# Optimization experiments

Hardware: AMD Instinct MI355X
Metric: run time of the kernel (lower is better)

Reference implementation:

```python
import jax, jax.numpy as jnp
import numpy as np

D_MODEL = 1024
NUM_HEADS = 16
D_INTERNAL = D_MODEL // NUM_HEADS
ROPE_BASE = 10000.0


def justnorm(x):
    return x / jnp.linalg.norm(x, axis=-1, keepdims=True)


def rotate_half(x):
    h = x.shape[-1] // 2
    return jnp.concatenate([-x[..., h:], x[..., :h]], axis=-1)


def setup_inputs() -> dict:
    key = jax.random.key(0)
    ks = jax.random.split(key, 8)
    B, T, dm, H, di = 4, 2048, D_MODEL, NUM_HEADS, D_INTERNAL
    x = jax.random.normal(ks[0], (B, T, dm), dtype=jnp.float32)
    stdev_h = 1.0 / (dm + di) ** 0.5
    qkv = jax.random.uniform(ks[1], (H, 3 * di, dm), minval=-stdev_h, maxval=stdev_h, dtype=jnp.float32)
    qkv = justnorm(qkv)  # per-row L2 normalization as in torch init
    sqk = (dm ** -0.5) * jnp.ones((H, di), dtype=jnp.float32)
    stdev = 1.0 / (4 * dm + dm) ** 0.5
    W_O = justnorm(jax.random.uniform(ks[2], (dm, dm), minval=-stdev, maxval=stdev, dtype=jnp.float32))
    Wu = justnorm(jax.random.uniform(ks[3], (8 * dm, dm), minval=-stdev, maxval=stdev, dtype=jnp.float32))
    Wv = justnorm(jax.random.uniform(ks[4], (dm, 4 * dm), minval=-stdev, maxval=stdev, dtype=jnp.float32))
    attn_alpha = (dm ** -0.5) * jnp.ones((dm,), dtype=jnp.float32)
    mlp_alpha = jnp.ones((dm,), dtype=jnp.float32)
    suv = jnp.ones((8 * dm,), dtype=jnp.float32)
    return {"x": x, "qkv": qkv, "sqk": sqk, "W_O": W_O, "Wu": Wu, "Wv": Wv,
            "attn_alpha": attn_alpha, "mlp_alpha": mlp_alpha, "suv": suv}


def _forward(x, qkv, sqk, W_O, Wu, Wv, attn_alpha, mlp_alpha, suv):
    B, T, dm = x.shape
    H = qkv.shape[0]
    di = qkv.shape[1] // 3
    sqrt_dm = jnp.sqrt(jnp.asarray(dm, x.dtype))
    # Per-head QKV projection, batched over heads: [B,H,T,3*di]
    qkv_out = jnp.einsum('btd,hed->bhte', x, qkv)
    Q, K, V = jnp.split(qkv_out, 3, axis=-1)
    # RoPE over full d_internal
    inv_freq = 1.0 / (ROPE_BASE ** (jnp.arange(0, di, 2, dtype=jnp.float32) / di))
    freqs = jnp.arange(T, dtype=jnp.float32)[:, None] * inv_freq[None, :]
    emb = jnp.concatenate([freqs, freqs], axis=-1)  # [T, di]
    cos, sin = jnp.cos(emb), jnp.sin(emb)
    Q = Q * cos + rotate_half(Q) * sin
    K = K * cos + rotate_half(K) * sin
    # sqk effective scale: sqk * (1.0 / d_model**-0.5)
    sqk_eff = sqk * sqrt_dm  # [H, di]
    Q = justnorm(Q) * sqk_eff[None, :, None, :]
    K = justnorm(K) * sqk_eff[None, :, None, :]
    # SDPA with non-standard scale = d_model**0.5, causal (eval mode)
    scores = jnp.einsum('bhqd,bhkd->bhqk', Q, K) * sqrt_dm
    causal = jnp.tril(jnp.ones((T, T), dtype=bool))
    scores = jnp.where(causal[None, None], scores, jnp.finfo(x.dtype).min)
    attn = jax.nn.softmax(scores, axis=-1)
    out = jnp.einsum('bhqk,bhkd->bhqd', attn, V)
    t = out.transpose(0, 2, 1, 3).reshape(B, T, dm)
    t = t @ W_O.T
    # nGPT-style attention lerp residual: attn_alpha * (0.05 / d_model**-0.5)
    lr = jnp.abs(attn_alpha * (0.05 * sqrt_dm))
    A = justnorm(x)
    Bn = justnorm(t)
    x1 = justnorm(A + lr * (Bn - A))
    # SwiGLU MLP
    uv = x1 @ Wu.T
    uv = (suv * sqrt_dm) * uv
    tn = justnorm(uv)
    u, v = jnp.split(tn, 2, axis=-1)
    res = u * jax.nn.silu(v)
    t = res @ Wv.T
    lr2 = jnp.abs(mlp_alpha * 0.05)
    A = justnorm(x1)
    Bn = justnorm(t)
    return justnorm(A + lr2 * (Bn - A))


def reference(x, qkv, sqk, W_O, Wu, Wv, attn_alpha, mlp_alpha, suv):
    return _forward(x, qkv, sqk, W_O, Wu, Wv, attn_alpha, mlp_alpha, suv)
```

## Files before the change

### kernel.cpp

```cpp
#include <hip/hip_runtime.h>
#include <hip/hip_bf16.h>


#define B_   4
#define T_   2048
#define DM   1024
#define H_   16
#define DI   64
#define NROW (B_ * T_)

using bf16 = __hip_bfloat16;
typedef __attribute__((ext_vector_type(8))) short bfrag;
typedef __attribute__((ext_vector_type(4))) float f4;

#define EXPB 46.166241f

__device__ __forceinline__ float ldf(const float* p) { return *p; }
__device__ __forceinline__ float ldf(const bf16* p)  { return __bfloat162float(*p); }
__device__ __forceinline__ void  stf(float* p, float v) { *p = v; }
__device__ __forceinline__ void  stf(bf16* p, float v)  { *p = __float2bfloat16(v); }

__device__ __forceinline__ unsigned short bfbits(float a) {
    bf16 h = __float2bfloat16(a);
    return __builtin_bit_cast(unsigned short, h);
}
__device__ __forceinline__ unsigned pk2(float a, float b) {
    return (unsigned)bfbits(a) | ((unsigned)bfbits(b) << 16);
}

__device__ __forceinline__ float fexp2(float x) {
    return __builtin_amdgcn_exp2f(x);
}

__device__ __forceinline__ float wave_sum(float v) {
#pragma unroll
    for (int off = 32; off; off >>= 1) v += __shfl_xor(v, off, 64);
    return v;
}

__device__ __forceinline__ float block_sum(float v) {
    __shared__ float sm[4];
    int lane = threadIdx.x & 63, w = threadIdx.x >> 6;
    v = wave_sum(v);
    __syncthreads();
    if (lane == 0) sm[w] = v;
    __syncthreads();
    return sm[0] + sm[1] + sm[2] + sm[3];
}

typedef __attribute__((address_space(1))) const void g_void;
typedef __attribute__((address_space(3))) void l_void;
__device__ __forceinline__ void gl_lds(const void* g, void* l) {
    __builtin_amdgcn_global_load_lds((g_void*)g, (l_void*)l, 16, 0, 0);
}

__global__ __launch_bounds__(256)
void f32_to_bf16_k(const float* __restrict__ in, bf16* __restrict__ out, long n)
{
    long i = ((long)blockIdx.x * 256 + threadIdx.x) * 8;
    if (i >= n) return;
    float4 a = *(const float4*)(in + i);
    float4 b = *(const float4*)(in + i + 4);
    union { bfrag f; unsigned u[4]; } o;
    o.u[0] = pk2(a.x, a.y); o.u[1] = pk2(a.z, a.w);
    o.u[2] = pk2(b.x, b.y); o.u[3] = pk2(b.z, b.w);
    *(bfrag*)(out + i) = o.f;
}

template <typename TC>
__global__ __launch_bounds__(256)
void gemm_bf16(const bf16* __restrict__ A, const bf16* __restrict__ Bm,
               TC* __restrict__ C, int M, int N, int K)
{
    __shared__ bf16 lds[2][2][128 * 32];
    const int tid  = threadIdx.x;
    const int w    = tid >> 6, lane = tid & 63;
    const int g    = lane >> 4, c = lane & 15;
    const int m0   = blockIdx.y * 128, n0 = blockIdx.x * 128;
    const int wm   = w >> 1, wn = w & 1;

    const int srow = (lane >> 2);
    const int skc  = 8 * (lane & 3);

    f4 acc[4][4] = {{{0,0,0,0}}};

    const int NT = K >> 5;

#pragma unroll
    for (int q = 0; q < 2; q++) {
        int cidx = w * 2 + q;
        int row  = 16 * cidx + srow;
        gl_lds(A + (long)(m0 + row) * K + skc, &lds[0][0][cidx * 512]);
        gl_lds(Bm + (long)(n0 + row) * K + skc, &lds[0][1][cidx * 512]);
    }
    __syncthreads();

    for (int t = 0; t < NT; t++) {
        int cur = t & 1;
        if (t + 1 < NT) {
            int k0 = (t + 1) << 5;
#pragma unroll
            for (int q = 0; q < 2; q++) {
                int cidx = w * 2 + q;
                int row  = 16 * cidx + srow;
                gl_lds(A + (long)(m0 + row) * K + k0 + skc, &lds[cur ^ 1][0][cidx * 512]);
                gl_lds(Bm + (long)(n0 + row) * K + k0 + skc, &lds[cur ^ 1][1][cidx * 512]);
            }
        }
        const bf16* bufA = &lds[cur][0][0];
        const bf16* bufB = &lds[cur][1][0];
        bfrag af[4], bb[4];
#pragma unroll
        for (int mi = 0; mi < 4; mi++)
            af[mi] = *(const bfrag*)(bufA + (64 * wm + 16 * mi + c) * 32 + 8 * g);
#pragma unroll
        for (int ni = 0; ni < 4; ni++)
            bb[ni] = *(const bfrag*)(bufB + (64 * wn + 16 * ni + c) * 32 + 8 * g);
#pragma unroll
        for (int mi = 0; mi < 4; mi++)
#pragma unroll
            for (int ni = 0; ni < 4; ni++)
                acc[mi][ni] = __builtin_amdgcn_mfma_f32_16x16x32_bf16(
                    af[mi], bb[ni], acc[mi][ni], 0, 0, 0);
        __syncthreads();
    }

#pragma unroll
    for (int mi = 0; mi < 4; mi++)
#pragma unroll
        for (int ni = 0; ni < 4; ni++) {
            long row = m0 + 64 * wm + 16 * mi + 4 * g;
            long col = n0 + 64 * wn + 16 * ni + c;
#pragma unroll
            for (int r = 0; r < 4; r++)
                stf(&C[(row + r) * N + col], acc[mi][ni][r]);
        }
}

template <typename TC>
__global__ __launch_bounds__(512, 2)
void gemm_bf16_256(const bf16* __restrict__ A, const bf16* __restrict__ Bm,
                   TC* __restrict__ C, int M, int N, int K)
{
    __shared__ bf16 lds[2][2][256 * 64];
    const int tid  = threadIdx.x;
    const int w    = tid >> 6, lane = tid & 63;
    const int g    = lane >> 4, c = lane & 15;
    const int m0   = blockIdx.y * 256, n0 = blockIdx.x * 256;
    const int wm   = w & 1, wn = w >> 1;
    const int srow8 = lane >> 3;
    const int swz   = 8 * ((lane & 7) ^ srow8);
    const int cx    = c & 7;

    f4 acc[8][4] = {{{0,0,0,0}}};

    const int NT = K >> 6;

    auto STAGE = [&](int buf, int t) {
        int k0 = t << 6;
#pragma unroll
        for (int i = 0; i < 4; i++) {
            int rb = w * 32 + i * 8;
            gl_lds(A  + (long)(m0 + rb + srow8) * K + k0 + swz, &lds[buf][0][rb * 64]);
            gl_lds(Bm + (long)(n0 + rb + srow8) * K + k0 + swz, &lds[buf][1][rb * 64]);
        }
    };

    STAGE(0, 0);
    STAGE(1, 1);
    asm volatile("s_waitcnt vmcnt(8)" ::: "memory");
    __builtin_amdgcn_s_barrier();

    for (int t = 0; t < NT; t++) {
        const bf16* bufA = &lds[t & 1][0][0];
        const bf16* bufB = &lds[t & 1][1][0];

        bfrag a0[4][2], b0[4][2];
#pragma unroll
        for (int mi = 0; mi < 4; mi++)
#pragma unroll
            for (int kk = 0; kk < 2; kk++)
                a0[mi][kk] = *(const bfrag*)(bufA + (wm * 128 + mi * 16 + c) * 64
                                                  + 8 * ((4 * kk + g) ^ cx));
#pragma unroll
        for (int ni = 0; ni < 4; ni++)
#pragma unroll
            for (int kk = 0; kk < 2; kk++)
                b0[ni][kk] = *(const bfrag*)(bufB + (wn * 64 + ni * 16 + c) * 64
                                                  + 8 * ((4 * kk + g) ^ cx));
        asm volatile("s_waitcnt lgkmcnt(0)" ::: "memory");
        __builtin_amdgcn_sched_barrier(0);
        __builtin_amdgcn_s_setprio(1);
#pragma unroll
        for (int mi = 0; mi < 4; mi++)
#pragma unroll
            for (int ni = 0; ni < 4; ni++) {
                acc[mi][ni] = __builtin_amdgcn_mfma_f32_16x16x32_bf16(
                    a0[mi][0], b0[ni][0], acc[mi][ni], 0, 0, 0);
                acc[mi][ni] = __builtin_amdgcn_mfma_f32_16x16x32_bf16(
                    a0[mi][1], b0[ni][1], acc[mi][ni], 0, 0, 0);
            }
        __builtin_amdgcn_s_setprio(0);

        bfrag a1[4][2];
#pragma unroll
        for (int mi = 0; mi < 4; mi++)
#pragma unroll
            for (int kk = 0; kk < 2; kk++)
                a1[mi][kk] = *(const bfrag*)(bufA + (wm * 128 + (mi + 4) * 16 + c) * 64
                                                  + 8 * ((4 * kk + g) ^ cx));
        asm volatile("s_waitcnt lgkmcnt(0)" ::: "memory");
        __builtin_amdgcn_sched_barrier(0);
        __builtin_amdgcn_s_setprio(1);
#pragma unroll
        for (int mi = 0; mi < 4; mi++)
#pragma unroll
            for (int ni = 0; ni < 4; ni++) {
                acc[mi + 4][ni] = __builtin_amdgcn_mfma_f32_16x16x32_bf16(
                    a1[mi][0], b0[ni][0], acc[mi + 4][ni], 0, 0, 0);
                acc[mi + 4][ni] = __builtin_amdgcn_mfma_f32_16x16x32_bf16(
                    a1[mi][1], b0[ni][1], acc[mi + 4][ni], 0, 0, 0);
            }
        __builtin_amdgcn_s_setprio(0);

        __builtin_amdgcn_s_barrier();
        if (t + 2 < NT) {
            STAGE(t & 1, t + 2);
            asm volatile("s_waitcnt vmcnt(8)" ::: "memory");
        } else if (t + 1 < NT) {
            asm volatile("s_waitcnt vmcnt(0)" ::: "memory");
        }
        __builtin_amdgcn_s_barrier();
    }

#pragma unroll
    for (int mi = 0; mi < 8; mi++)
#pragma unroll
        for (int ni = 0; ni < 4; ni++) {
            long row = m0 + wm * 128 + mi * 16 + 4 * g;
            long col = n0 + wn * 64 + ni * 16 + c;
#pragma unroll
            for (int r = 0; r < 4; r++)
                stf(&C[(row + r) * N + col], acc[mi][ni][r]);
        }
}

__global__ __launch_bounds__(256)
void rope_norm_qk(const bf16* __restrict__ QKVb, const float* __restrict__ sqk,
                  bf16* __restrict__ Qb, bf16* __restrict__ Kb, bf16* __restrict__ Vt)
{
    int gw   = (blockIdx.x * 256 + threadIdx.x) >> 6;
    int lane = threadIdx.x & 63;
    int h = gw / NROW, row = gw % NROW, t = row % T_, b = row / T_;

    const bf16* base = QKVb + (long)row * 3072 + h * 192;
    float q = __bfloat162float(base[lane]);
    float k = __bfloat162float(base[64 + lane]);
    bf16  v = base[128 + lane];

    int   j   = lane & 31;
    float inv = expf(-(float)j * (9.210340371976184f / 32.f));
    float ang = (float)t * inv;
    float s = sinf(ang), cc = cosf(ang);

    float qp = __shfl_xor(q, 32, 64);
    float kp = __shfl_xor(k, 32, 64);
    float sgn = (lane < 32) ? -1.f : 1.f;
    float qr = q * cc + sgn * qp * s;
    float kr = k * cc + sgn * kp * s;

    float qs = wave_sum(qr * qr);
    float ks = wave_sum(kr * kr);
    float se = sqk[h * 64 + lane] * 32.f;

    long idx = ((long)h * NROW + row) * 64 + lane;
    Qb[idx] = __float2bfloat16(qr * rsqrtf(qs) * se * EXPB);
    Kb[idx] = __float2bfloat16(kr * rsqrtf(ks) * se);
    Vt[((long)(h * B_ + b) * 64 + lane) * T_ + t] = v;
}

__global__ __launch_bounds__(256)
void attn_mfma(const bf16* __restrict__ Qb, const bf16* __restrict__ Kb,
               const bf16* __restrict__ Vt, bf16* __restrict__ O)
{
    __shared__ bf16 kv[2][2][64 * 64];

    int orig   = blockIdx.x;
    int xcd    = orig & 7;
    int rest   = orig >> 3;
    int bh     = xcd * 8 + (rest & 7);
    int blkraw = rest >> 3;
    int blk    = (blkraw & 1) ? (15 - (blkraw >> 1)) : (blkraw >> 1);
    int w      = threadIdx.x >> 6;
    int pr     = blk * 4 + w;
    int h = bh >> 2, b = bh & 3;

    int lane = threadIdx.x & 63;
    int g = lane >> 4, c = lane & 15;

    const bf16* kbase = Kb + ((long)h * NROW + (long)b * T_) * 64;
    const bf16* vbase = Vt + (long)(h * B_ + b) * 64 * (long)T_;

    int q0A = pr * 16, q0B = (127 - pr) * 16;
    const bf16* qbA = Qb + ((long)h * NROW + (long)b * T_ + q0A) * 64;
    const bf16* qbB = Qb + ((long)h * NROW + (long)b * T_ + q0B) * 64;
    bfrag qfA0 = *(const bfrag*)(qbA + (long)c * 64 + 8 * g);
    bfrag qfA1 = *(const bfrag*)(qbA + (long)c * 64 + 32 + 8 * g);
    bfrag qfB0 = *(const bfrag*)(qbB + (long)c * 64 + 8 * g);
    bfrag qfB1 = *(const bfrag*)(qbB + (long)c * 64 + 32 + 8 * g);

    const f4 CINIT = {-EXPB, -EXPB, -EXPB, -EXPB};

    f4 otA[4] = {{0,0,0,0},{0,0,0,0},{0,0,0,0},{0,0,0,0}};
    f4 otB[4] = {{0,0,0,0},{0,0,0,0},{0,0,0,0},{0,0,0,0}};
    float lA = 0.f, lB = 0.f;

    const int nA = blk, nB = 31 - blk, KT = nB;
    int qgA = q0A + c, qgB = q0B + c;

    const int srow8  = lane >> 3;
    const int swz    = 8 * ((lane & 7) ^ srow8);

    auto STAGE = [&](int buf, int kt) {
        int k0 = kt * 64;
#pragma unroll
        for (int i = 0; i < 2; i++) {
            int rb  = (w * 2 + i) * 8;
            int row = rb + srow8;
            gl_lds(kbase + (long)(k0 + row) * 64 + swz, &kv[buf][0][rb * 64]);
            gl_lds(vbase + (long)row * T_ + k0 + swz,   &kv[buf][1][rb * 64]);
        }
    };

    STAGE(0, 0);
    __syncthreads();

    const int cx = c & 7;

    for (int kt = 0; kt <= KT; kt++) {
        int buf = kt & 1;
        if (kt < KT) STAGE(buf ^ 1, kt + 1);

        const bf16* Kl = &kv[buf][0][0];
        const bf16* Vl = &kv[buf][1][0];
        int k0 = kt * 64;
        bool actA = (kt <= nA);
        unsigned wvA[8], wvB[8];

#pragma unroll
        for (int kb = 0; kb < 4; kb++) {
            const bf16* kr = Kl + (16 * kb + c) * 64;
            bfrag ka = *(const bfrag*)(kr + 8 * (g ^ cx));
            bfrag kc = *(const bfrag*)(kr + 8 * ((g | 4) ^ cx));

            f4 sB = __builtin_amdgcn_mfma_f32_16x16x32_bf16(ka, qfB0, CINIT, 0, 0, 0);
            sB = __builtin_amdgcn_mfma_f32_16x16x32_bf16(kc, qfB1, sB, 0, 0, 0);
            if (kt == nB) {
#pragma unroll
                for (int r = 0; r < 4; r++)
                    if (k0 + 16 * kb + 4 * g + r > qgB) sB[r] = -1e30f;
            }
            float eB0 = fexp2(sB[0]), eB1 = fexp2(sB[1]);
            float eB2 = fexp2(sB[2]), eB3 = fexp2(sB[3]);
            lB += (eB0 + eB1) + (eB2 + eB3);
            wvB[2 * kb]     = pk2(eB0, eB1);
            wvB[2 * kb + 1] = pk2(eB2, eB3);

            if (actA) {
                f4 sA = __builtin_amdgcn_mfma_f32_16x16x32_bf16(ka, qfA0, CINIT, 0, 0, 0);
                sA = __builtin_amdgcn_mfma_f32_16x16x32_bf16(kc, qfA1, sA, 0, 0, 0);
                if (kt == nA) {
#pragma unroll
                    for (int r = 0; r < 4; r++)
                        if (k0 + 16 * kb + 4 * g + r > qgA) sA[r] = -1e30f;
                }
                float eA0 = fexp2(sA[0]), eA1 = fexp2(sA[1]);
                float eA2 = fexp2(sA[2]), eA3 = fexp2(sA[3]);
                lA += (eA0 + eA1) + (eA2 + eA3);
                wvA[2 * kb]     = pk2(eA0, eA1);
                wvA[2 * kb + 1] = pk2(eA2, eA3);
            }
        }

#pragma unroll
        for (int p = 0; p < 2; p++) {
            int s0l = c + 32 * (g & 1), s1l = s0l + 16;
            bool hi = (g >= 2);

            unsigned Bb0 = (unsigned)__shfl((int)wvB[4 * p + 0], s0l, 64);
            unsigned Bb1 = (unsigned)__shfl((int)wvB[4 * p + 1], s0l, 64);
            unsigned Bb2 = (unsigned)__shfl((int)wvB[4 * p + 2], s0l, 64);
            unsigned Bb3 = (unsigned)__shfl((int)wvB[4 * p + 3], s0l, 64);
            unsigned Bb4 = (unsigned)__shfl((int)wvB[4 * p + 0], s1l, 64);
            unsigned Bb5 = (unsigned)__shfl((int)wvB[4 * p + 1], s1l, 64);
            unsigned Bb6 = (unsigned)__shfl((int)wvB[4 * p + 2], s1l, 64);
            unsigned Bb7 = (unsigned)__shfl((int)wvB[4 * p + 3], s1l, 64);
            union { bfrag f; unsigned u[4]; } pfB;
            pfB.u[0] = hi ? Bb2 : Bb0;
            pfB.u[1] = hi ? Bb3 : Bb1;
            pfB.u[2] = hi ? Bb6 : Bb4;
            pfB.u[3] = hi ? Bb7 : Bb5;

            union { bfrag f; unsigned u[4]; } pfA;
            if (actA) {
                unsigned Ab0 = (unsigned)__shfl((int)wvA[4 * p + 0], s0l, 64);
                unsigned Ab1 = (unsigned)__shfl((int)wvA[4 * p + 1], s0l, 64);
                unsigned Ab2 = (unsigned)__shfl((int)wvA[4 * p + 2], s0l, 64);
                unsigned Ab3 = (unsigned)__shfl((int)wvA[4 * p + 3], s0l, 64);
                unsigned Ab4 = (unsigned)__shfl((int)wvA[4 * p + 0], s1l, 64);
                unsigned Ab5 = (unsigned)__shfl((int)wvA[4 * p + 1], s1l, 64);
                unsigned Ab6 = (unsigned)__shfl((int)wvA[4 * p + 2], s1l, 64);
                unsigned Ab7 = (unsigned)__shfl((int)wvA[4 * p + 3], s1l, 64);
                pfA.u[0] = hi ? Ab2 : Ab0;
                pfA.u[1] = hi ? Ab3 : Ab1;
                pfA.u[2] = hi ? Ab6 : Ab4;
                pfA.u[3] = hi ? Ab7 : Ab5;
            }

#pragma unroll
            for (int dblk = 0; dblk < 4; dblk++) {
                bfrag vf = *(const bfrag*)(Vl + (16 * dblk + c) * 64
                                              + 8 * (((p << 2) | g) ^ cx));
                otB[dblk] = __builtin_amdgcn_mfma_f32_16x16x32_bf16(vf, pfB.f, otB[dblk], 0, 0, 0);
                if (actA)
                    otA[dblk] = __builtin_amdgcn_mfma_f32_16x16x32_bf16(vf, pfA.f, otA[dblk], 0, 0, 0);
            }
        }
        __syncthreads();
    }

    lA += __shfl_xor(lA, 16, 64); lA += __shfl_xor(lA, 32, 64);
    lB += __shfl_xor(lB, 16, 64); lB += __shfl_xor(lB, 32, 64);

    float invA = 1.f / lA, invB = 1.f / lB;
    long orowA = (long)(b * T_ + q0A + c) * DM + h * 64;
    long orowB = (long)(b * T_ + q0B + c) * DM + h * 64;
#pragma unroll
    for (int dblk = 0; dblk < 4; dblk++)
#pragma unroll
        for (int r = 0; r < 4; r++) {
            O[orowA + 16 * dblk + 4 * g + r] = __float2bfloat16(otA[dblk][r] * invA);
            O[orowB + 16 * dblk + 4 * g + r] = __float2bfloat16(otB[dblk][r] * invB);
        }
}

template <typename TT>
__global__ __launch_bounds__(256)
void lerp_norm(const float* __restrict__ X, const TT* __restrict__ Tt,
               const float* __restrict__ alpha, float ascale,
               float* __restrict__ Out, bf16* __restrict__ OutB)
{
    long row = blockIdx.x;
    const float* xr = X  + row * DM;
    const TT*    tr = Tt + row * DM;
    int tid = threadIdx.x;

    float xs[4], ts[4], sx = 0.f, st = 0.f;
#pragma unroll
    for (int i = 0; i < 4; i++) {
        int d = tid + 256 * i;
        xs[i] = xr[d]; ts[i] = ldf(&tr[d]);
        sx += xs[i] * xs[i]; st += ts[i] * ts[i];
    }
    sx = block_sum(sx);
    st = block_sum(st);
    float ix = rsqrtf(sx), it = rsqrtf(st);

    float ys[4], sy = 0.f;
#pragma unroll
    for (int i = 0; i < 4; i++) {
        int d = tid + 256 * i;
        float a  = xs[i] * ix;
        float bn = ts[i] * it;
        float lr = fabsf(alpha[d] * ascale);
        ys[i] = a + lr * (bn - a);
        sy += ys[i] * ys[i];
    }
    sy = block_sum(sy);
    float iy = rsqrtf(sy);
#pragma unroll
    for (int i = 0; i < 4; i++) {
        int d = tid + 256 * i;
        float o = ys[i] * iy;
        Out[row * DM + d] = o;
        if (OutB) OutB[row * DM + d] = __float2bfloat16(o);
    }
}

__global__ __launch_bounds__(256)
void mlp_act(const bf16* __restrict__ UV, const float* __restrict__ suv,
             bf16* __restrict__ R)
{
    long row = blockIdx.x;
    const bf16* ur = UV + row * 8192;
    int tid = threadIdx.x;

    float ss = 0.f;
#pragma unroll
    for (int i = 0; i < 32; i++) {
        int j = tid + 256 * i;
        float v = __bfloat162float(ur[j]) * suv[j] * 32.f;
        ss += v * v;
    }
    ss = block_sum(ss);
    float inv = rsqrtf(ss);

#pragma unroll
    for (int i = 0; i < 16; i++) {
        int j = tid + 256 * i;
        float u = __bfloat162float(ur[j])        * suv[j]        * 32.f * inv;
        float v = __bfloat162float(ur[4096 + j]) * suv[4096 + j] * 32.f * inv;
        float sil = v / (1.f + __expf(-v));
        R[row * 4096 + j] = __float2bfloat16(u * sil);
    }
}

extern "C" void kernel_launch(void* const* d_in, const int* in_sizes, int n_in,
                              void* d_out, int out_size, void* d_ws, size_t ws_size,
                              hipStream_t stream)
{
    const float* x          = (const float*)d_in[0];
    const float* qkv_w      = (const float*)d_in[1];
    const float* sqk        = (const float*)d_in[2];
    const float* W_O        = (const float*)d_in[3];
    const float* Wu         = (const float*)d_in[4];
    const float* Wv         = (const float*)d_in[5];
    const float* attn_alpha = (const float*)d_in[6];
    const float* mlp_alpha  = (const float*)d_in[7];
    const float* suv        = (const float*)d_in[8];
    float* out = (float*)d_out;

    const long MiB = 1048576;
    char* ws = (char*)d_ws;
    float* x1    = (float*)(ws + 0 * MiB);
    bf16*  x1b   = (bf16*) (ws + 32 * MiB);
    bf16*  QKVb  = (bf16*) (ws + 48 * MiB);
    bf16*  tbuf  = (bf16*) (ws + 48 * MiB);
    bf16*  uv    = (bf16*) (ws + 48 * MiB);
    bf16*  t2    = (bf16*) (ws + 48 * MiB);
    bf16*  xb    = (bf16*) (ws + 144 * MiB);
    bf16*  Qb    = (bf16*) (ws + 144 * MiB);
    bf16*  Wub   = (bf16*) (ws + 144 * MiB);
    bf16*  Kb    = (bf16*) (ws + 160 * MiB);
    bf16*  Vt    = (bf16*) (ws + 176 * MiB);
    bf16*  Wvb   = (bf16*) (ws + 176 * MiB);
    bf16*  res   = (bf16*) (ws + 112 * MiB);
    bf16*  qkvwb = (bf16*) (ws + 192 * MiB);
    bf16*  attno = (bf16*) (ws + 192 * MiB);
    bf16*  Wob   = (bf16*) (ws + 208 * MiB);

    f32_to_bf16_k<<<4096, 256, 0, stream>>>(x, xb, 8388608L);
    f32_to_bf16_k<<<1536, 256, 0, stream>>>(qkv_w, qkvwb, 3145728L);
    f32_to_bf16_k<<<512,  256, 0, stream>>>(W_O, Wob, 1048576L);

    gemm_bf16_256<bf16><<<dim3(12, 32), 512, 0, stream>>>(xb, qkvwb, QKVb, NROW, 3072, DM);

    rope_norm_qk<<<(H_ * NROW) / 4, 256, 0, stream>>>(QKVb, sqk, Qb, Kb, Vt);

    attn_mfma<<<1024, 256, 0, stream>>>(Qb, Kb, Vt, attno);

    gemm_bf16<bf16><<<dim3(8, 64), 256, 0, stream>>>(attno, Wob, tbuf, NROW, DM, DM);

    lerp_norm<bf16><<<NROW, 256, 0, stream>>>(x, tbuf, attn_alpha, 1.6f, x1, x1b);

    f32_to_bf16_k<<<4096, 256, 0, stream>>>(Wu, Wub, 8388608L);
    f32_to_bf16_k<<<2048, 256, 0, stream>>>(Wv, Wvb, 4194304L);

    for (int half = 0; half < 2; half++) {
        gemm_bf16_256<bf16><<<dim3(32, 16), 512, 0, stream>>>(
            x1b + (long)half * 4096 * DM, Wub, uv, 4096, 8 * DM, DM);
        mlp_act<<<4096, 256, 0, stream>>>(uv, suv, res + (long)half * 4096 * 4096);
    }

    gemm_bf16<bf16><<<dim3(8, 64), 256, 0, stream>>>(res, Wvb, t2, NROW, DM, 4 * DM);

    lerp_norm<bf16><<<NROW, 256, 0, stream>>>(x1, t2, mlp_alpha, 0.05f, out, (bf16*)nullptr);
}
```

Before: 581.9 us.

## Interleave attention query-tile assignment across warps and drop fp32 x1 buffer

Attention blocks now assign each warp a query pair strided by 16 instead of four adjacent pairs. Each warp gets its own A/B causal limits, the block loops to the longest warp's limit, and MFMA work is skipped for warps past their range, aiming to balance work across blocks. Separately, the first lerp_norm no longer writes a fp32 x1 buffer, and the final lerp_norm reads the bf16 x1b copy instead, cutting memory traffic. The cost is some precision loss in the residual path, plus idle warps inside a block when limits differ.

```diff
diff --git a/kernel.cpp b/kernel.cpp
--- a/kernel.cpp
+++ b/kernel.cpp
@@ -289,10 +289,9 @@
     int xcd    = orig & 7;
     int rest   = orig >> 3;
     int bh     = xcd * 8 + (rest & 7);
-    int blkraw = rest >> 3;
-    int blk    = (blkraw & 1) ? (15 - (blkraw >> 1)) : (blkraw >> 1);
+    int j      = rest >> 3;
     int w      = threadIdx.x >> 6;
-    int pr     = blk * 4 + w;
+    int pr     = j + 16 * w;
     int h = bh >> 2, b = bh & 3;
 
     int lane = threadIdx.x & 63;
@@ -315,7 +314,9 @@
     f4 otB[4] = {{0,0,0,0},{0,0,0,0},{0,0,0,0},{0,0,0,0}};
     float lA = 0.f, lB = 0.f;
 
-    const int nA = blk, nB = 31 - blk, KT = nB;
+    const int nA = pr >> 2;
+    const int nB = 31 - nA;
+    const int KTblk = 31 - (j >> 2);
     int qgA = q0A + c, qgB = q0B + c;
 
     const int srow8  = lane >> 3;
@@ -337,93 +338,99 @@
 
     const int cx = c & 7;
 
-    for (int kt = 0; kt <= KT; kt++) {
+    for (int kt = 0; kt <= KTblk; kt++) {
         int buf = kt & 1;
-        if (kt < KT) STAGE(buf ^ 1, kt + 1);
+        if (kt < KTblk) STAGE(buf ^ 1, kt + 1);
 
         const bf16* Kl = &kv[buf][0][0];
         const bf16* Vl = &kv[buf][1][0];
         int k0 = kt * 64;
         bool actA = (kt <= nA);
+        bool actB = (kt <= nB);
         unsigned wvA[8], wvB[8];
 
-#pragma unroll
-        for (int kb = 0; kb < 4; kb++) {
-            const bf16* kr = Kl + (16 * kb + c) * 64;
-            bfrag ka = *(const bfrag*)(kr + 8 * (g ^ cx));
-            bfrag kc = *(const bfrag*)(kr + 8 * ((g | 4) ^ cx));
-
-            f4 sB = __builtin_amdgcn_mfma_f32_16x16x32_bf16(ka, qfB0, CINIT, 0, 0, 0);
-            sB = __builtin_amdgcn_mfma_f32_16x16x32_bf16(kc, qfB1, sB, 0, 0, 0);
-            if (kt == nB) {
-#pragma unroll
-                for (int r = 0; r < 4; r++)
-                    if (k0 + 16 * kb + 4 * g + r > qgB) sB[r] = -1e30f;
+        if (actB || actA) {
+#pragma unroll
+            for (int kb = 0; kb < 4; kb++) {
+                const bf16* kr = Kl + (16 * kb + c) * 64;
+                bfrag ka = *(const bfrag*)(kr + 8 * (g ^ cx));
+                bfrag kc = *(const bfrag*)(kr + 8 * ((g | 4) ^ cx));
+
+                if (actB) {
+                    f4 sB = __builtin_amdgcn_mfma_f32_16x16x32_bf16(ka, qfB0, CINIT, 0, 0, 0);
+                    sB = __builtin_amdgcn_mfma_f32_16x16x32_bf16(kc, qfB1, sB, 0, 0, 0);
+                    if (kt == nB) {
+#pragma unroll
+                        for (int r = 0; r < 4; r++)
+                            if (k0 + 16 * kb + 4 * g + r > qgB) sB[r] = -1e30f;
+                    }
+                    float eB0 = fexp2(sB[0]), eB1 = fexp2(sB[1]);
+                    float eB2 = fexp2(sB[2]), eB3 = fexp2(sB[3]);
+                    lB += (eB0 + eB1) + (eB2 + eB3);
+                    wvB[2 * kb]     = pk2(eB0, eB1);
+                    wvB[2 * kb + 1] = pk2(eB2, eB3);
+                }
+
+                if (actA) {
+                    f4 sA = __builtin_amdgcn_mfma_f32_16x16x32_bf16(ka, qfA0, CINIT, 0, 0, 0);
+                    sA = __builtin_amdgcn_mfma_f32_16x16x32_bf16(kc, qfA1, sA, 0, 0, 0);
+                    if (kt == nA) {
+#pragma unroll
+                        for (int r = 0; r < 4; r++)
+                            if (k0 + 16 * kb + 4 * g + r > qgA) sA[r] = -1e30f;
+                    }
+                    float eA0 = fexp2(sA[0]), eA1 = fexp2(sA[1]);
+                    float eA2 = fexp2(sA[2]), eA3 = fexp2(sA[3]);
+                    lA += (eA0 + eA1) + (eA2 + eA3);
+                    wvA[2 * kb]     = pk2(eA0, eA1);
+                    wvA[2 * kb + 1] = pk2(eA2, eA3);
+                }
             }
-            float eB0 = fexp2(sB[0]), eB1 = fexp2(sB[1]);
-            float eB2 = fexp2(sB[2]), eB3 = fexp2(sB[3]);
-            lB += (eB0 + eB1) + (eB2 + eB3);
-            wvB[2 * kb]     = pk2(eB0, eB1);
-            wvB[2 * kb + 1] = pk2(eB2, eB3);
-
-            if (actA) {
-                f4 sA = __builtin_amdgcn_mfma_f32_16x16x32_bf16(ka, qfA0, CINIT, 0, 0, 0);
-                sA = __builtin_amdgcn_mfma_f32_16x16x32_bf16(kc, qfA1, sA, 0, 0, 0);
-                if (kt == nA) {
-#pragma unroll
-                    for (int r = 0; r < 4; r++)
-                        if (k0 + 16 * kb + 4 * g + r > qgA) sA[r] = -1e30f;
+
+#pragma unroll
+            for (int p = 0; p < 2; p++) {
+                int s0l = c + 32 * (g & 1), s1l = s0l + 16;
+                bool hi = (g >= 2);
+
+                union { bfrag f; unsigned u[4]; } pfB, pfA;
+                if (actB) {
+                    unsigned Bb0 = (unsigned)__shfl((int)wvB[4 * p + 0], s0l, 64);
+                    unsigned Bb1 = (unsigned)__shfl((int)wvB[4 * p + 1], s0l, 64);
+                    unsigned Bb2 = (unsigned)__shfl((int)wvB[4 * p + 2], s0l, 64);
+                    unsigned Bb3 = (unsigned)__shfl((int)wvB[4 * p + 3], s0l, 64);
+                    unsigned Bb4 = (unsigned)__shfl((int)wvB[4 * p + 0], s1l, 64);
+                    unsigned Bb5 = (unsigned)__shfl((int)wvB[4 * p + 1], s1l, 64);
+                    unsigned Bb6 = (unsigned)__shfl((int)wvB[4 * p + 2], s1l, 64);
+                    unsigned Bb7 = (unsigned)__shfl((int)wvB[4 * p + 3], s1l, 64);
+                    pfB.u[0] = hi ? Bb2 : Bb0;
+                    pfB.u[1] = hi ? Bb3 : Bb1;
+                    pfB.u[2] = hi ? Bb6 : Bb4;
+                    pfB.u[3] = hi ? Bb7 : Bb5;
                 }
-                float eA0 = fexp2(sA[0]), eA1 = fexp2(sA[1]);
-                float eA2 = fexp2(sA[2]), eA3 = fexp2(sA[3]);
-                lA += (eA0 + eA1) + (eA2 + eA3);
-                wvA[2 * kb]     = pk2(eA0, eA1);
-                wvA[2 * kb + 1] = pk2(eA2, eA3);
-            }
-        }
-
-#pragma unroll
-        for (int p = 0; p < 2; p++) {
-            int s0l = c + 32 * (g & 1), s1l = s0l + 16;
-            bool hi = (g >= 2);
-
-            unsigned Bb0 = (unsigned)__shfl((int)wvB[4 * p + 0], s0l, 64);
-            unsigned Bb1 = (unsigned)__shfl((int)wvB[4 * p + 1], s0l, 64);
-            unsigned Bb2 = (unsigned)__shfl((int)wvB[4 * p + 2], s0l, 64);
-            unsigned Bb3 = (unsigned)__shfl((int)wvB[4 * p + 3], s0l, 64);
-            unsigned Bb4 = (unsigned)__shfl((int)wvB[4 * p + 0], s1l, 64);
-            unsigned Bb5 = (unsigned)__shfl((int)wvB[4 * p + 1], s1l, 64);
-            unsigned Bb6 = (unsigned)__shfl((int)wvB[4 * p + 2], s1l, 64);
-            unsigned Bb7 = (unsigned)__shfl((int)wvB[4 * p + 3], s1l, 64);
-            union { bfrag f; unsigned u[4]; } pfB;
-            pfB.u[0] = hi ? Bb2 : Bb0;
-            pfB.u[1] = hi ? Bb3 : Bb1;
-            pfB.u[2] = hi ? Bb6 : Bb4;
-            pfB.u[3] = hi ? Bb7 : Bb5;
-
-            union { bfrag f; unsigned u[4]; } pfA;
-            if (actA) {
-                unsigned Ab0 = (unsigned)__shfl((int)wvA[4 * p + 0], s0l, 64);
-                unsigned Ab1 = (unsigned)__shfl((int)wvA[4 * p + 1], s0l, 64);
-                unsigned Ab2 = (unsigned)__shfl((int)wvA[4 * p + 2], s0l, 64);
-                unsigned Ab3 = (unsigned)__shfl((int)wvA[4 * p + 3], s0l, 64);
-                unsigned Ab4 = (unsigned)__shfl((int)wvA[4 * p + 0], s1l, 64);
-                unsigned Ab5 = (unsigned)__shfl((int)wvA[4 * p + 1], s1l, 64);
-                unsigned Ab6 = (unsigned)__shfl((int)wvA[4 * p + 2], s1l, 64);
-                unsigned Ab7 = (unsigned)__shfl((int)wvA[4 * p + 3], s1l, 64);
-                pfA.u[0] = hi ? Ab2 : Ab0;
-                pfA.u[1] = hi ? Ab3 : Ab1;
-                pfA.u[2] = hi ? Ab6 : Ab4;
-                pfA.u[3] = hi ? Ab7 : Ab5;
-            }
-
-#pragma unroll
-            for (int dblk = 0; dblk < 4; dblk++) {
-                bfrag vf = *(const bfrag*)(Vl + (16 * dblk + c) * 64
-                                              + 8 * (((p << 2) | g) ^ cx));
-                otB[dblk] = __builtin_amdgcn_mfma_f32_16x16x32_bf16(vf, pfB.f, otB[dblk], 0, 0, 0);
-                if (actA)
-                    otA[dblk] = __builtin_amdgcn_mfma_f32_16x16x32_bf16(vf, pfA.f, otA[dblk], 0, 0, 0);
+                if (actA) {
+                    unsigned Ab0 = (unsigned)__shfl((int)wvA[4 * p + 0], s0l, 64);
+                    unsigned Ab1 = (unsigned)__shfl((int)wvA[4 * p + 1], s0l, 64);
+                    unsigned Ab2 = (unsigned)__shfl((int)wvA[4 * p + 2], s0l, 64);
+                    unsigned Ab3 = (unsigned)__shfl((int)wvA[4 * p + 3], s0l, 64);
+                    unsigned Ab4 = (unsigned)__shfl((int)wvA[4 * p + 0], s1l, 64);
+                    unsigned Ab5 = (unsigned)__shfl((int)wvA[4 * p + 1], s1l, 64);
+                    unsigned Ab6 = (unsigned)__shfl((int)wvA[4 * p + 2], s1l, 64);
+                    unsigned Ab7 = (unsigned)__shfl((int)wvA[4 * p + 3], s1l, 64);
+                    pfA.u[0] = hi ? Ab2 : Ab0;
+                    pfA.u[1] = hi ? Ab3 : Ab1;
+                    pfA.u[2] = hi ? Ab6 : Ab4;
+                    pfA.u[3] = hi ? Ab7 : Ab5;
+                }
+
+#pragma unroll
+                for (int dblk = 0; dblk < 4; dblk++) {
+                    bfrag vf = *(const bfrag*)(Vl + (16 * dblk + c) * 64
+                                                  + 8 * (((p << 2) | g) ^ cx));
+                    if (actB)
+                        otB[dblk] = __builtin_amdgcn_mfma_f32_16x16x32_bf16(vf, pfB.f, otB[dblk], 0, 0, 0);
+                    if (actA)
+                        otA[dblk] = __builtin_amdgcn_mfma_f32_16x16x32_bf16(vf, pfA.f, otA[dblk], 0, 0, 0);
+                }
             }
         }
         __syncthreads();
@@ -444,22 +451,22 @@
         }
 }
 
-template <typename TT>
+template <typename TX, typename TT>
 __global__ __launch_bounds__(256)
-void lerp_norm(const float* __restrict__ X, const TT* __restrict__ Tt,
+void lerp_norm(const TX* __restrict__ X, const TT* __restrict__ Tt,
                const float* __restrict__ alpha, float ascale,
-               float* __restrict__ Out, bf16* __restrict__ OutB)
+               float* __restrict__ OutF, bf16* __restrict__ OutB)
 {
     long row = blockIdx.x;
-    const float* xr = X  + row * DM;
-    const TT*    tr = Tt + row * DM;
+    const TX* xr = X  + row * DM;
+    const TT* tr = Tt + row * DM;
     int tid = threadIdx.x;
 
     float xs[4], ts[4], sx = 0.f, st = 0.f;
 #pragma unroll
     for (int i = 0; i < 4; i++) {
         int d = tid + 256 * i;
-        xs[i] = xr[d]; ts[i] = ldf(&tr[d]);
+        xs[i] = ldf(&xr[d]); ts[i] = ldf(&tr[d]);
         sx += xs[i] * xs[i]; st += ts[i] * ts[i];
     }
     sx = block_sum(sx);
@@ -482,7 +489,7 @@
     for (int i = 0; i < 4; i++) {
         int d = tid + 256 * i;
         float o = ys[i] * iy;
-        Out[row * DM + d] = o;
+        if (OutF) OutF[row * DM + d] = o;
         if (OutB) OutB[row * DM + d] = __float2bfloat16(o);
     }
 }
@@ -532,7 +539,6 @@
 
     const long MiB = 1048576;
     char* ws = (char*)d_ws;
-    float* x1    = (float*)(ws + 0 * MiB);
     bf16*  x1b   = (bf16*) (ws + 32 * MiB);
     bf16*  QKVb  = (bf16*) (ws + 48 * MiB);
     bf16*  tbuf  = (bf16*) (ws + 48 * MiB);
@@ -561,7 +567,8 @@
 
     gemm_bf16<bf16><<<dim3(8, 64), 256, 0, stream>>>(attno, Wob, tbuf, NROW, DM, DM);
 
-    lerp_norm<bf16><<<NROW, 256, 0, stream>>>(x, tbuf, attn_alpha, 1.6f, x1, x1b);
+    lerp_norm<float, bf16><<<NROW, 256, 0, stream>>>(x, tbuf, attn_alpha, 1.6f,
+                                                     (float*)nullptr, x1b);
 
     f32_to_bf16_k<<<4096, 256, 0, stream>>>(Wu, Wub, 8388608L);
     f32_to_bf16_k<<<2048, 256, 0, stream>>>(Wv, Wvb, 4194304L);
@@ -574,5 +581,6 @@
 
     gemm_bf16<bf16><<<dim3(8, 64), 256, 0, stream>>>(res, Wvb, t2, NROW, DM, 4 * DM);
 
-    lerp_norm<bf16><<<NROW, 256, 0, stream>>>(x1, t2, mlp_alpha, 0.05f, out, (bf16*)nullptr);
-}
+    lerp_norm<bf16, bf16><<<NROW, 256, 0, stream>>>(x1b, t2, mlp_alpha, 0.05f,
+                                                    out, (bf16*)nullptr);
+}
```

After: 627.1 us. 7.8% more time.
